# Kernel tuning notes

Hardware: AMD Instinct MI355X
Metric: run time of the kernel (lower is better)

## Reference

```python
import jax, jax.numpy as jnp
import numpy as np

COMMA_ID = 1010   # BERT wordpiece id for ','
H, NH, HD = 768, 8, 96
B, S = 64, 512
NSEG = 17         # 16 commas per row -> 17 segments
EPS = 1e-5


def setup_inputs() -> dict:
    key = jax.random.key(0)
    ks = jax.random.split(key, 16)
    text_hs = jax.random.normal(ks[0], (B, S, H), jnp.float32)
    cols_hs = jax.random.normal(ks[1], (B, S, H), jnp.float32)
    ids = jax.random.randint(ks[2], (B, S), 0, 30522)
    ids = jnp.where(ids == COMMA_ID, COMMA_ID + 1, ids)  # avoid accidental commas
    comma_pos = jnp.arange(16, 257, 16)                  # 16 commas per row
    ids = ids.at[:, comma_pos].set(COMMA_ID)
    sc = 0.02
    wq = jax.random.normal(ks[3], (H, H), jnp.float32) * sc
    wk = jax.random.normal(ks[4], (H, H), jnp.float32) * sc
    wv = jax.random.normal(ks[5], (H, H), jnp.float32) * sc
    bq = jnp.zeros((H,), jnp.float32)
    bk = jnp.zeros((H,), jnp.float32)
    bv = jnp.zeros((H,), jnp.float32)
    wo = jax.random.normal(ks[6], (H, H), jnp.float32) * sc
    bo = jnp.zeros((H,), jnp.float32)
    gamma = jnp.ones((H,), jnp.float32)
    beta = jnp.zeros((H,), jnp.float32)
    w_out = jax.random.normal(ks[7], (1, H), jnp.float32) * sc
    b_out = jnp.zeros((1,), jnp.float32)
    return dict(text_hs=text_hs, cols_hs=cols_hs, wq=wq, wk=wk, wv=wv,
                bq=bq, bk=bk, bv=bv, wo=wo, bo=bo, gamma=gamma, beta=beta,
                w_out=w_out, b_out=b_out, columns_input_ids=ids, n_segments=NSEG)


def _forward(text_hs, cols_hs, wq, wk, wv, bq, bk, bv, wo, bo,
             gamma, beta, w_out, b_out, columns_input_ids, n_segments):
    t = text_hs[:, 1:, :]   # drop first token, as in forward()  [B, L, H]
    c = cols_hs[:, 1:, :]
    L = t.shape[1]
    # --- nn.MultiheadAttention(query=cols, key=value=text), batch_first ---
    q = c @ wq.T + bq
    k = t @ wk.T + bk
    v = t @ wv.T + bv
    split = lambda x: x.reshape(x.shape[0], -1, NH, HD).transpose(0, 2, 1, 3)
    scores = jnp.einsum('bhqd,bhkd->bhqk', split(q), split(k)) / np.sqrt(HD).astype(np.float32)
    attn = jax.nn.softmax(scores, axis=-1)
    ctx = jnp.einsum('bhqk,bhkd->bhqd', attn, split(v))
    ctx = ctx.transpose(0, 2, 1, 3).reshape(c.shape[0], L, H)
    attn_out = ctx @ wo.T + bo
    # --- BatchNorm1d over channels (training-mode batch stats) ---
    xt = attn_out.transpose(0, 2, 1)            # [B, H, L]
    mu = xt.mean(axis=(0, 2), keepdims=True)
    var = xt.var(axis=(0, 2), keepdims=True)     # biased, as torch BN normalization
    xn = (xt - mu) / jnp.sqrt(var + EPS) * gamma[None, :, None] + beta[None, :, None]
    cross_out = c + xn.transpose(0, 2, 1)       # residual add
    fv = (cross_out @ w_out.T + b_out).squeeze(-1)   # [B, L] scores per token
    # --- compose_outputs: mean-pool comma-delimited ragged spans ---
    is_comma = columns_input_ids[:, :L] == COMMA_ID
    seg = jnp.cumsum(is_comma.astype(jnp.int32), axis=1) - is_comma.astype(jnp.int32)
    mask = (jnp.arange(L)[None, :] >= 1) & (~is_comma)    # slice_start=1, commas excluded
    oh = ((seg[:, :, None] == jnp.arange(n_segments)[None, None, :])
          & mask[:, :, None]).astype(fv.dtype)            # [B, L, J]
    sums = jnp.einsum('blj,bl->bj', oh, fv)
    cnt = oh.sum(axis=1)
    return sums / jnp.maximum(cnt, 1.0)                   # [B, n_segments]


def reference(text_hs, cols_hs, wq, wk, wv, bq, bk, bv, wo, bo,
              gamma, beta, w_out, b_out, columns_input_ids, n_segments):
    return _forward(text_hs, cols_hs, wq, wk, wv, bq, bk, bv, wo, bo,
                    gamma, beta, w_out, b_out, columns_input_ids, n_segments)
```

## Files before the change

kernel.cpp:

```cpp
#include <hip/hip_runtime.h>
#include <hip/hip_bf16.h>

#define COMMA_IDC 1010
#define NHEAD 8
#define Ll 511
#define Mrows 32704
#define NSEG 17

typedef __attribute__((ext_vector_type(8))) short bf16x8;
typedef __attribute__((ext_vector_type(4))) float f32x4;
typedef unsigned short u16;
typedef unsigned int u32;
typedef unsigned long long u64;

__device__ __forceinline__ u16 f2b(float f) {
  __hip_bfloat16 h = __float2bfloat16(f);
  return *reinterpret_cast<u16*>(&h);
}
__device__ __forceinline__ float b2f(u16 u) {
  u32 x = ((u32)u) << 16;
  return __builtin_bit_cast(float, x);
}

__device__ __forceinline__ void gld_lds16(const void* g, void* l) {
  __builtin_amdgcn_global_load_lds(
      (const __attribute__((address_space(1))) void*)(u64)g,
      (__attribute__((address_space(3))) void*)(u32)(u64)l,
      16, 0, 0);
}

#define MFMA16(a, b, c) __builtin_amdgcn_mfma_f32_16x16x32_bf16(a, b, c, 0, 0, 0)

__global__ void conv_sliced2(const float4* __restrict__ s0, const float4* __restrict__ s1,
                             ushort4* __restrict__ d0, ushort4* __restrict__ d1) {
  const float4* src = blockIdx.z ? s1 : s0;
  ushort4* dst = blockIdx.z ? d1 : d0;
  int b = blockIdx.y;
  int idx = blockIdx.x * 256 + threadIdx.x;
  if (idx >= Ll * 192) return;
  int l = idx / 192, c = idx - l * 192;
  float4 v = src[(b * 512 + l + 1) * 192 + c];
  ushort4 o; o.x = f2b(v.x); o.y = f2b(v.y); o.z = f2b(v.z); o.w = f2b(v.w);
  dst[(b * Ll + l) * 192 + c] = o;
}

__global__ void conv_w(const float4* __restrict__ wq, const float4* __restrict__ wk,
                       const float4* __restrict__ wv, const float4* __restrict__ wo,
                       ushort4* __restrict__ wqkvb, ushort4* __restrict__ wob) {
  int i = blockIdx.x * 256 + threadIdx.x;
  int seg = i / 147456, off = i - seg * 147456;
  const float4* s = (seg == 0) ? wq : ((seg == 1) ? wk : ((seg == 2) ? wv : wo));
  ushort4* d = (seg == 3) ? wob : (wqkvb + seg * 147456);
  float4 v = s[off];
  ushort4 o; o.x = f2b(v.x); o.y = f2b(v.y); o.z = f2b(v.z); o.w = f2b(v.w);
  d[off] = o;
}

__global__ void zero_kernel(float* p, int n) {
  int i = blockIdx.x * 256 + threadIdx.x;
  if (i < n) p[i] = 0.f;
}

#define LDA_(i, kk) (*(const bf16x8*)(sMem + bA + ((i) * 16 + fr) * 64 + ((((kk) * 4 + fq) ^ xm) << 3)))
#define LDW_(j, kk) (*(const bf16x8*)(sMem + bW + (((wc * 64 + (j) * 16) >> 7) * 8192) + \
                     (((wc * 64 + (j) * 16) & 127) + fr) * 64 + ((((kk) * 4 + fq) ^ xm) << 3)))
#define LGKM0 do { asm volatile("s_waitcnt lgkmcnt(0)" ::: "memory"); __builtin_amdgcn_sched_barrier(0); } while (0)

template<int NTILES, int NOUT, int QNT>
__global__ __launch_bounds__(512, 2) void gemm256(
    const u16* __restrict__ A0, const u16* __restrict__ A1, const u16* __restrict__ W,
    const float* __restrict__ b0, const float* __restrict__ b1, const float* __restrict__ b2,
    u16* __restrict__ outp)
{
  __shared__ __align__(16) u16 sMem[65536];
  const int tid = threadIdx.x;
  const int lane = tid & 63, wid = tid >> 6;
  const int fr = lane & 15, fq = lane >> 4;
  const int wr = wid >> 2, wc = wid & 3;
  const int xm = fr & 7;

  int fid = blockIdx.x;
  int xcd = fid & 7, w = fid >> 3;
  int mrow = xcd * 16 + w / NTILES;
  int ncol = w - (w / NTILES) * NTILES;
  const int m0 = mrow * 256, n0 = ncol * 256;
  const u16* __restrict__ A = (ncol < QNT) ? A0 : A1;

  const int rS = tid >> 3;
  const int cS = (tid & 7) ^ (rS & 7);
  const u16* gA0 = A + (u64)(m0 + rS) * 768 + cS * 8;
  const u16* gA1 = A + (u64)(m0 + 128 + rS) * 768 + cS * 8;
  const u16* gW0 = W + (u64)(n0 + rS) * 768 + cS * 8;
  const u16* gW1 = W + (u64)(n0 + 128 + rS) * 768 + cS * 8;
  const u32 st0 = tid * 8;

  f32x4 acc[8][4] = {};

  auto stage_all = [&](int buf, int kt) {
    const int kb = kt * 64;
    const u32 db = (u32)buf * 32768;
    gld_lds16(gA0 + kb, sMem + db + st0);
    gld_lds16(gA0 + kb + 49152, sMem + db + st0 + 4096);
    gld_lds16(gA1 + kb, sMem + db + 8192 + st0);
    gld_lds16(gA1 + kb + 49152, sMem + db + 8192 + st0 + 4096);
    gld_lds16(gW0 + kb, sMem + db + 16384 + st0);
    gld_lds16(gW0 + kb + 49152, sMem + db + 16384 + st0 + 4096);
    gld_lds16(gW1 + kb, sMem + db + 24576 + st0);
    gld_lds16(gW1 + kb + 49152, sMem + db + 24576 + st0 + 4096);
  };

  stage_all(0, 0);
  asm volatile("s_waitcnt vmcnt(0)" ::: "memory");
  __builtin_amdgcn_s_barrier();

  for (int kt = 0; kt < 12; ++kt) {
    const u32 db = (u32)(kt & 1) * 32768;
    const u32 bA = db + wr * 8192;
    const u32 bW = db + 16384;
    bf16x8 af[4][2], wf[2][2];

#pragma unroll
    for (int i = 0; i < 4; i++) { af[i][0] = LDA_(i, 0); af[i][1] = LDA_(i, 1); }
#pragma unroll
    for (int j = 0; j < 2; j++) { wf[j][0] = LDW_(j, 0); wf[j][1] = LDW_(j, 1); }
    __builtin_amdgcn_s_barrier();
    if (kt + 1 < 12) stage_all((kt + 1) & 1, kt + 1);
    LGKM0;
    __builtin_amdgcn_s_setprio(1);
#pragma unroll
    for (int i = 0; i < 4; i++)
#pragma unroll
      for (int j = 0; j < 2; j++) {
        acc[i][j] = MFMA16(af[i][0], wf[j][0], acc[i][j]);
        acc[i][j] = MFMA16(af[i][1], wf[j][1], acc[i][j]);
      }
    __builtin_amdgcn_s_setprio(0);
    __builtin_amdgcn_s_barrier();

#pragma unroll
    for (int j = 0; j < 2; j++) { wf[j][0] = LDW_(j + 2, 0); wf[j][1] = LDW_(j + 2, 1); }
    __builtin_amdgcn_s_barrier();
    LGKM0;
    __builtin_amdgcn_s_setprio(1);
#pragma unroll
    for (int i = 0; i < 4; i++)
#pragma unroll
      for (int j = 0; j < 2; j++) {
        acc[i][j + 2] = MFMA16(af[i][0], wf[j][0], acc[i][j + 2]);
        acc[i][j + 2] = MFMA16(af[i][1], wf[j][1], acc[i][j + 2]);
      }
    __builtin_amdgcn_s_setprio(0);
    __builtin_amdgcn_s_barrier();

#pragma unroll
    for (int i = 0; i < 4; i++) { af[i][0] = LDA_(i + 4, 0); af[i][1] = LDA_(i + 4, 1); }
#pragma unroll
    for (int j = 0; j < 2; j++) { wf[j][0] = LDW_(j, 0); wf[j][1] = LDW_(j, 1); }
    __builtin_amdgcn_s_barrier();
    LGKM0;
    __builtin_amdgcn_s_setprio(1);
#pragma unroll
    for (int i = 0; i < 4; i++)
#pragma unroll
      for (int j = 0; j < 2; j++) {
        acc[i + 4][j] = MFMA16(af[i][0], wf[j][0], acc[i + 4][j]);
        acc[i + 4][j] = MFMA16(af[i][1], wf[j][1], acc[i + 4][j]);
      }
    __builtin_amdgcn_s_setprio(0);
    __builtin_amdgcn_s_barrier();

#pragma unroll
    for (int j = 0; j < 2; j++) { wf[j][0] = LDW_(j + 2, 0); wf[j][1] = LDW_(j + 2, 1); }
    __builtin_amdgcn_s_barrier();
    LGKM0;
    __builtin_amdgcn_s_setprio(1);
#pragma unroll
    for (int i = 0; i < 4; i++)
#pragma unroll
      for (int j = 0; j < 2; j++) {
        acc[i + 4][j + 2] = MFMA16(af[i][0], wf[j][0], acc[i + 4][j + 2]);
        acc[i + 4][j + 2] = MFMA16(af[i][1], wf[j][1], acc[i + 4][j + 2]);
      }
    __builtin_amdgcn_s_setprio(0);
    asm volatile("s_waitcnt vmcnt(0)" ::: "memory");
    __builtin_amdgcn_s_barrier();
  }

  const float* bp = (n0 < 768) ? b0 : ((n0 < 1536) ? b1 : b2);
  const int bcol = n0 & 767;
  float bj[4];
#pragma unroll
  for (int j = 0; j < 4; j++) bj[j] = bp[bcol + wc * 64 + j * 16 + fr];

#pragma unroll
  for (int h = 0; h < 2; h++) {
    __syncthreads();
    if (wr == h) {
#pragma unroll
      for (int i = 0; i < 8; i++)
#pragma unroll
        for (int j = 0; j < 4; j++)
#pragma unroll
          for (int r = 0; r < 4; r++)
            sMem[(i * 16 + fq * 4 + r) * 264 + wc * 64 + j * 16 + fr] = f2b(acc[i][j][r] + bj[j]);
    }
    __syncthreads();
#pragma unroll
    for (int it = 0; it < 8; it++) {
      int chunk = tid + it * 512;
      int lr = chunk >> 5, ch = chunk & 31;
      *(bf16x8*)(outp + (u64)(m0 + h * 128 + lr) * NOUT + n0 + ch * 8) =
          *(const bf16x8*)(sMem + lr * 264 + ch * 8);
    }
  }
}

__global__ __launch_bounds__(256) void vtrans(const u16* __restrict__ QKV, u16* __restrict__ VT) {
  __shared__ __align__(16) u16 sT[128 * 128];
  int bh = blockIdx.y;
  int b = bh >> 3, h = bh & 7;
  int l0 = blockIdx.x * 128;
  u16* outp = VT + (u64)bh * 96 * 512;
  int t = threadIdx.x;
#pragma unroll
  for (int k = 0; k < 6; k++) {
    int c = t + k * 256;
    int l = c / 12, ch = c - l * 12;
    int lc = l0 + l; if (lc > 510) lc = 510;
    bf16x8 v = *(const bf16x8*)(QKV + (u64)(b * 511 + lc) * 2304 + 1536 + h * 96 + ch * 8);
    int chunk = l * 16 + (ch ^ ((l >> 3) & 7));
    *(bf16x8*)(sT + chunk * 8) = v;
  }
  __syncthreads();
#pragma unroll
  for (int k = 0; k < 6; k++) {
    int c = t + k * 256;
    int d = c >> 4, lch = c & 15;
    u16 vals[8];
#pragma unroll
    for (int k2 = 0; k2 < 8; k2++) {
      int r = lch * 8 + k2;
      int idx = r * 128 + (((d >> 3) ^ (lch & 7)) << 3) + (d & 7);
      vals[k2] = sT[idx];
    }
    bf16x8 o;
#pragma unroll
    for (int k2 = 0; k2 < 8; k2++) o[k2] = (short)vals[k2];
    *(bf16x8*)(outp + (u64)d * 512 + l0 + lch * 8) = o;
  }
}

#define PST 36
__global__ __launch_bounds__(256) void attn_kernel(
    const u16* __restrict__ QKV, const u16* __restrict__ VT, u16* __restrict__ ctxb)
{
  __shared__ __align__(16) u16 sK[32 * 96];
  __shared__ __align__(16) u16 sV[32 * 96];
  __shared__ __align__(16) u16 sP[4][16 * PST];
  const int tid = threadIdx.x, lane = tid & 63, wid = tid >> 6;
  int fid = blockIdx.x;
  int xcd = fid & 7, slot = (fid >> 3) & 3, grp = fid >> 5;
  int bh = grp * 8 + xcd;
  int b = bh >> 3, h = bh & 7;
  int q0 = slot * 128;
  const int fr = lane & 15, fq = lane >> 4;
  const u64 mb = (u64)(b * 511);
  const u64 hbV = (u64)bh * 96 * 512;

  bf16x8 qf[2][3];
#pragma unroll
  for (int sub = 0; sub < 2; sub++) {
    int qr = q0 + wid * 32 + sub * 16 + fr; if (qr > 510) qr = 510;
#pragma unroll
    for (int ks = 0; ks < 3; ks++)
      qf[sub][ks] = *(const bf16x8*)(QKV + (mb + qr) * 2304 + h * 96 + ks * 32 + fq * 8);
  }

  f32x4 ctx[2][6] = {};
  f32x4 sumP[2] = {};

  int cK1 = wid * 64 + lane;
  int kr1 = cK1 / 12, kc1 = cK1 - kr1 * 12;
  const u16* gK1 = QKV + (mb + kr1) * 2304 + 768 + h * 96 + kc1 * 8;
  int cK2 = 256 + cK1;
  int kr2 = cK2 / 12, kc2 = cK2 - kr2 * 12;
  const u16* gK2 = QKV + (mb + kr2) * 2304 + 768 + h * 96 + kc2 * 8;
  int cV1 = wid * 64 + lane;
  int dV1 = cV1 >> 2, jV1 = (cV1 & 3) ^ ((dV1 >> 1) & 3);
  const u16* gV1 = VT + hbV + (u64)dV1 * 512 + jV1 * 8;
  int cV2 = 256 + (wid - 2) * 64 + lane;
  int dV2 = cV2 >> 2, jV2 = (cV2 & 3) ^ ((dV2 >> 1) & 3);
  const u16* gV2 = VT + hbV + (u64)dV2 * 512 + jV2 * 8;

  u16* lK1 = sK + (u32)(wid * 64) * 8;
  u16* lK2 = sK + (u32)(256 + wid * 64) * 8;
  u16* lV1 = sV + (u32)(wid * 64) * 8;
  u16* lV2 = sV + (u32)(256 + (wid - 2) * 64) * 8;
  u16* pw = &sP[wid][0];

  const float cs = 0.10206207261596575f;
  const int cpx = fq ^ ((fr >> 1) & 3);

  for (int kv0 = 0; kv0 < 511; kv0 += 32) {
    __syncthreads();
    gld_lds16(gK1, lK1); gK1 += (u64)32 * 2304;
    if (wid < 2) { gld_lds16(gK2, lK2); gK2 += (u64)32 * 2304; }
    gld_lds16(gV1, lV1); gV1 += 32;
    if (wid >= 2) { gld_lds16(gV2, lV2); gV2 += 32; }
    __syncthreads();

    bf16x8 kf0[3], kf1[3];
#pragma unroll
    for (int ks = 0; ks < 3; ks++) {
      kf0[ks] = *(const bf16x8*)(sK + fr * 96 + ks * 32 + fq * 8);
      kf1[ks] = *(const bf16x8*)(sK + (16 + fr) * 96 + ks * 32 + fq * 8);
    }
    const bool ok1 = (kv0 + 16 + fr) < Ll;

#pragma unroll
    for (int sub = 0; sub < 2; sub++) {
      f32x4 s0 = {}, s1 = {};
#pragma unroll
      for (int ks = 0; ks < 3; ks++) {
        s0 = MFMA16(qf[sub][ks], kf0[ks], s0);
        s1 = MFMA16(qf[sub][ks], kf1[ks], s1);
      }
      float p0[4], p1[4];
#pragma unroll
      for (int r = 0; r < 4; r++) {
        p0[r] = __expf(s0[r] * cs);
        float e1 = __expf(s1[r] * cs);
        p1[r] = ok1 ? e1 : 0.f;
        sumP[sub][r] += p0[r] + p1[r];
      }
#pragma unroll
      for (int r = 0; r < 4; r++) {
        int row = fq * 4 + r;
        pw[row * PST + fr] = f2b(p0[r]);
        pw[row * PST + 16 + fr] = f2b(p1[r]);
      }
      bf16x8 pf = *(const bf16x8*)(pw + fr * PST + fq * 8);
#pragma unroll
      for (int df = 0; df < 6; df++) {
        bf16x8 vf = *(const bf16x8*)(sV + (df * 16 + fr) * 32 + cpx * 8);
        ctx[sub][df] = MFMA16(pf, vf, ctx[sub][df]);
      }
    }
  }

#pragma unroll
  for (int sub = 0; sub < 2; sub++) {
    float inv[4];
#pragma unroll
    for (int r = 0; r < 4; r++) {
      float s = sumP[sub][r];
      s += __shfl_xor(s, 1, 64);
      s += __shfl_xor(s, 2, 64);
      s += __shfl_xor(s, 4, 64);
      s += __shfl_xor(s, 8, 64);
      inv[r] = 1.f / s;
    }
#pragma unroll
    for (int df = 0; df < 6; df++) {
#pragma unroll
      for (int r = 0; r < 4; r++) {
        int q = q0 + wid * 32 + sub * 16 + fq * 4 + r;
        if (q < Ll)
          ctxb[(u64)(b * Ll + q) * 768 + h * 96 + df * 16 + fr] = f2b(ctx[sub][df][r] * inv[r]);
      }
    }
  }
}

__global__ __launch_bounds__(256) void stats_kernel(const u16* __restrict__ ao,
                                                    float* __restrict__ ssum, float* __restrict__ ssq)
{
  int t = threadIdx.x;
  int row0 = blockIdx.x * 128;
  int rowEnd = row0 + 128; if (rowEnd > Mrows) rowEnd = Mrows;
  float s[3] = {0.f, 0.f, 0.f}, q[3] = {0.f, 0.f, 0.f};
  for (int m = row0; m < rowEnd; m++) {
    const u16* rp = ao + (u64)m * 768;
#pragma unroll
    for (int i = 0; i < 3; i++) {
      float v = b2f(rp[t + i * 256]);
      s[i] += v; q[i] += v * v;
    }
  }
#pragma unroll
  for (int i = 0; i < 3; i++) {
    atomicAdd(&ssum[t + i * 256], s[i]);
    atomicAdd(&ssq[t + i * 256], q[i]);
  }
}

__global__ __launch_bounds__(256) void derived_kernel(
    const float* __restrict__ ssum, const float* __restrict__ ssq,
    const float* __restrict__ w_out, const float* __restrict__ b_out,
    const float* __restrict__ gamma, const float* __restrict__ beta,
    float* __restrict__ weff, float* __restrict__ consts)
{
  __shared__ float red[256];
  int t = threadIdx.x;
  float acc = 0.f;
  const float invN = 1.f / 32704.f;
#pragma unroll
  for (int i = 0; i < 3; i++) {
    int hh = t + i * 256;
    float mu = ssum[hh] * invN;
    float var = ssq[hh] * invN - mu * mu;
    float rstd = 1.f / sqrtf(var + 1e-5f);
    float we = w_out[hh] * gamma[hh] * rstd;
    weff[hh] = we;
    acc += w_out[hh] * beta[hh] - we * mu;
  }
  red[t] = acc; __syncthreads();
  for (int s = 128; s > 0; s >>= 1) { if (t < s) red[t] += red[t + s]; __syncthreads(); }
  if (t == 0) consts[0] = b_out[0] + red[0];
}

__global__ __launch_bounds__(256) void fv_kernel(
    const u16* __restrict__ ao, const u16* __restrict__ cb,
    const float* __restrict__ w_out, const float* __restrict__ weff,
    const float* __restrict__ consts, float* __restrict__ fv)
{
  int lane = threadIdx.x & 63, wid = threadIdx.x >> 6;
  int m = blockIdx.x * 4 + wid;
  if (m >= Mrows) return;
  const u16* ap = ao + (u64)m * 768;
  const u16* cp = cb + (u64)m * 768;
  float acc = 0.f;
#pragma unroll
  for (int i = 0; i < 12; i++) {
    int hh = lane + i * 64;
    acc += b2f(ap[hh]) * weff[hh] + b2f(cp[hh]) * w_out[hh];
  }
#pragma unroll
  for (int off = 1; off < 64; off <<= 1) acc += __shfl_xor(acc, off, 64);
  if (lane == 0) fv[m] = acc + consts[0];
}

__global__ __launch_bounds__(64) void seg_kernel(
    const float* __restrict__ fv, const int* __restrict__ ids, float* __restrict__ out)
{
  __shared__ float ssum[NSEG];
  __shared__ int scnt[NSEG];
  int lane = threadIdx.x;
  int b = blockIdx.x;
  if (lane < NSEG) { ssum[lane] = 0.f; scnt[lane] = 0; }
  __syncthreads();
  int carry = 0;
  for (int it = 0; it < 8; it++) {
    int l = it * 64 + lane;
    bool active = l < Ll;
    int id = active ? ids[b * 512 + l] : 0;
    bool comma = active && (id == COMMA_IDC);
    u64 cmask = __ballot(comma);
    int seg = carry + __popcll(cmask & ((1ull << lane) - 1ull));
    bool valid = active && (l >= 1) && !comma;
    if (valid && seg < NSEG) {
      atomicAdd(&ssum[seg], fv[b * Ll + l]);
      atomicAdd(&scnt[seg], 1);
    }
    carry += __popcll(cmask);
  }
  __syncthreads();
  if (lane < NSEG) {
    float c = (float)scnt[lane];
    out[b * NSEG + lane] = ssum[lane] / fmaxf(c, 1.f);
  }
}

extern "C" void kernel_launch(void* const* d_in, const int* in_sizes, int n_in,
                              void* d_out, int out_size, void* d_ws, size_t ws_size,
                              hipStream_t stream)
{
  const float* text  = (const float*)d_in[0];
  const float* cols  = (const float*)d_in[1];
  const float* wq    = (const float*)d_in[2];
  const float* wk    = (const float*)d_in[3];
  const float* wvp   = (const float*)d_in[4];
  const float* bq    = (const float*)d_in[5];
  const float* bk    = (const float*)d_in[6];
  const float* bv    = (const float*)d_in[7];
  const float* wo    = (const float*)d_in[8];
  const float* bo    = (const float*)d_in[9];
  const float* gamma = (const float*)d_in[10];
  const float* beta  = (const float*)d_in[11];
  const float* w_out = (const float*)d_in[12];
  const float* b_out = (const float*)d_in[13];
  const int*   ids   = (const int*)d_in[14];
  float* out = (float*)d_out;

  char* ws = (char*)d_ws;
  u16* cb    = (u16*)(ws + 0ull);
  u16* tb    = (u16*)(ws + 50331648ull);
  u16* wqkvb = (u16*)(ws + 100663296ull);
  u16* wob   = (u16*)(ws + 104202240ull);
  u16* QKVb  = (u16*)(ws + 105381888ull);
  u16* ctxb  = (u16*)(ws + 256376832ull);
  u16* VTb   = tb;
  u16* aob   = QKVb;
  float* ssum   = (float*)(ws + 105381888ull + 50331648ull);
  float* ssq    = ssum + 768;
  float* weff   = ssum + 1536;
  float* consts = ssum + 2304;
  float* fv     = (float*)((char*)ssum + 16384ull);

  conv_sliced2<<<dim3(384, 64, 2), 256, 0, stream>>>(
      (const float4*)cols, (const float4*)text, (ushort4*)cb, (ushort4*)tb);
  conv_w<<<2304, 256, 0, stream>>>(
      (const float4*)wq, (const float4*)wk, (const float4*)wvp, (const float4*)wo,
      (ushort4*)wqkvb, (ushort4*)wob);

  gemm256<9, 2304, 3><<<1152, 512, 0, stream>>>(cb, tb, wqkvb, bq, bk, bv, QKVb);
  vtrans<<<dim3(4, 512), 256, 0, stream>>>(QKVb, VTb);
  attn_kernel<<<2048, 256, 0, stream>>>(QKVb, VTb, ctxb);

  zero_kernel<<<6, 256, 0, stream>>>(ssum, 1536);
  gemm256<3, 768, 99><<<384, 512, 0, stream>>>(ctxb, ctxb, wob, bo, bo, bo, aob);
  stats_kernel<<<256, 256, 0, stream>>>(aob, ssum, ssq);
  derived_kernel<<<1, 256, 0, stream>>>(ssum, ssq, w_out, b_out, gamma, beta, weff, consts);
  fv_kernel<<<8176, 256, 0, stream>>>(aob, cb, w_out, weff, consts, fv);
  seg_kernel<<<64, 64, 0, stream>>>(fv, ids, out);
}
```

Before: 460.2 us.

## Software-pipeline GEMM LDS fragment loads with MFMA using double register sets

Restructures the bf16 GEMM main loop so LDS fragment reads for the next sub-block are issued while MFMAs on the previous fragments run. Two register sets (A/B) are used, and the last quadrant's MFMAs are carried into the next iteration and an epilogue. Most per-quadrant s_barriers and explicit lgkmcnt waits are removed. The aim is to hide LDS latency and cut synchronisation stalls, at the cost of more VGPRs (possible spilling under launch bounds 512,2) and reliance on compiler-inserted waits.

```diff
diff --git a/kernel.cpp b/kernel.cpp
--- a/kernel.cpp
+++ b/kernel.cpp
@@ -30,6 +30,7 @@
 }
 
 #define MFMA16(a, b, c) __builtin_amdgcn_mfma_f32_16x16x32_bf16(a, b, c, 0, 0, 0)
+#define SBAR0 __builtin_amdgcn_sched_barrier(0)
 
 __global__ void conv_sliced2(const float4* __restrict__ s0, const float4* __restrict__ s1,
                              ushort4* __restrict__ d0, ushort4* __restrict__ d1) {
@@ -61,10 +62,9 @@
   if (i < n) p[i] = 0.f;
 }
 
-#define LDA_(i, kk) (*(const bf16x8*)(sMem + bA + ((i) * 16 + fr) * 64 + ((((kk) * 4 + fq) ^ xm) << 3)))
-#define LDW_(j, kk) (*(const bf16x8*)(sMem + bW + (((wc * 64 + (j) * 16) >> 7) * 8192) + \
+#define LDA(db, i, kk) (*(const bf16x8*)(sMem + (db) + wr * 8192 + ((i) * 16 + fr) * 64 + ((((kk) * 4 + fq) ^ xm) << 3)))
+#define LDW(db, j, kk) (*(const bf16x8*)(sMem + (db) + 16384 + (((wc * 64 + (j) * 16) >> 7) * 8192) + \
                      (((wc * 64 + (j) * 16) & 127) + fr) * 64 + ((((kk) * 4 + fq) ^ xm) << 3)))
-#define LGKM0 do { asm volatile("s_waitcnt lgkmcnt(0)" ::: "memory"); __builtin_amdgcn_sched_barrier(0); } while (0)
 
 template<int NTILES, int NOUT, int QNT>
 __global__ __launch_bounds__(512, 2) void gemm256(
@@ -95,6 +95,7 @@
   const u32 st0 = tid * 8;
 
   f32x4 acc[8][4] = {};
+  bf16x8 afA[4][2], afB[4][2], wfA[2][2], wfB[2][2];
 
   auto stage_all = [&](int buf, int kt) {
     const int kb = kt * 64;
@@ -110,80 +111,87 @@
   };
 
   stage_all(0, 0);
-  asm volatile("s_waitcnt vmcnt(0)" ::: "memory");
-  __builtin_amdgcn_s_barrier();
 
   for (int kt = 0; kt < 12; ++kt) {
     const u32 db = (u32)(kt & 1) * 32768;
-    const u32 bA = db + wr * 8192;
-    const u32 bW = db + 16384;
-    bf16x8 af[4][2], wf[2][2];
-
-#pragma unroll
-    for (int i = 0; i < 4; i++) { af[i][0] = LDA_(i, 0); af[i][1] = LDA_(i, 1); }
-#pragma unroll
-    for (int j = 0; j < 2; j++) { wf[j][0] = LDW_(j, 0); wf[j][1] = LDW_(j, 1); }
+
+    asm volatile("s_waitcnt vmcnt(0)" ::: "memory");
+    SBAR0;
     __builtin_amdgcn_s_barrier();
+    SBAR0;
+#pragma unroll
+    for (int i = 0; i < 4; i++) { afA[i][0] = LDA(db, i, 0); afA[i][1] = LDA(db, i, 1); }
+#pragma unroll
+    for (int j = 0; j < 2; j++) { wfA[j][0] = LDW(db, j, 0); wfA[j][1] = LDW(db, j, 1); }
+    if (kt > 0) {
+      __builtin_amdgcn_s_setprio(1);
+#pragma unroll
+      for (int i = 0; i < 4; i++)
+#pragma unroll
+        for (int j = 0; j < 2; j++) {
+          acc[i + 4][j + 2] = MFMA16(afB[i][0], wfB[j][0], acc[i + 4][j + 2]);
+          acc[i + 4][j + 2] = MFMA16(afB[i][1], wfB[j][1], acc[i + 4][j + 2]);
+        }
+      __builtin_amdgcn_s_setprio(0);
+    }
+    SBAR0;
+    __builtin_amdgcn_s_barrier();
+    SBAR0;
     if (kt + 1 < 12) stage_all((kt + 1) & 1, kt + 1);
-    LGKM0;
+    SBAR0;
+
+#pragma unroll
+    for (int j = 0; j < 2; j++) { wfB[j][0] = LDW(db, j + 2, 0); wfB[j][1] = LDW(db, j + 2, 1); }
     __builtin_amdgcn_s_setprio(1);
 #pragma unroll
     for (int i = 0; i < 4; i++)
 #pragma unroll
       for (int j = 0; j < 2; j++) {
-        acc[i][j] = MFMA16(af[i][0], wf[j][0], acc[i][j]);
-        acc[i][j] = MFMA16(af[i][1], wf[j][1], acc[i][j]);
+        acc[i][j] = MFMA16(afA[i][0], wfA[j][0], acc[i][j]);
+        acc[i][j] = MFMA16(afA[i][1], wfA[j][1], acc[i][j]);
       }
     __builtin_amdgcn_s_setprio(0);
-    __builtin_amdgcn_s_barrier();
-
-#pragma unroll
-    for (int j = 0; j < 2; j++) { wf[j][0] = LDW_(j + 2, 0); wf[j][1] = LDW_(j + 2, 1); }
-    __builtin_amdgcn_s_barrier();
-    LGKM0;
+    SBAR0;
+
+#pragma unroll
+    for (int i = 0; i < 4; i++) { afB[i][0] = LDA(db, i + 4, 0); afB[i][1] = LDA(db, i + 4, 1); }
+#pragma unroll
+    for (int j = 0; j < 2; j++) { wfA[j][0] = LDW(db, j, 0); wfA[j][1] = LDW(db, j, 1); }
     __builtin_amdgcn_s_setprio(1);
 #pragma unroll
     for (int i = 0; i < 4; i++)
 #pragma unroll
       for (int j = 0; j < 2; j++) {
-        acc[i][j + 2] = MFMA16(af[i][0], wf[j][0], acc[i][j + 2]);
-        acc[i][j + 2] = MFMA16(af[i][1], wf[j][1], acc[i][j + 2]);
+        acc[i][j + 2] = MFMA16(afA[i][0], wfB[j][0], acc[i][j + 2]);
+        acc[i][j + 2] = MFMA16(afA[i][1], wfB[j][1], acc[i][j + 2]);
       }
     __builtin_amdgcn_s_setprio(0);
-    __builtin_amdgcn_s_barrier();
-
-#pragma unroll
-    for (int i = 0; i < 4; i++) { af[i][0] = LDA_(i + 4, 0); af[i][1] = LDA_(i + 4, 1); }
-#pragma unroll
-    for (int j = 0; j < 2; j++) { wf[j][0] = LDW_(j, 0); wf[j][1] = LDW_(j, 1); }
-    __builtin_amdgcn_s_barrier();
-    LGKM0;
+    SBAR0;
+
+#pragma unroll
+    for (int j = 0; j < 2; j++) { wfB[j][0] = LDW(db, j + 2, 0); wfB[j][1] = LDW(db, j + 2, 1); }
     __builtin_amdgcn_s_setprio(1);
 #pragma unroll
     for (int i = 0; i < 4; i++)
 #pragma unroll
       for (int j = 0; j < 2; j++) {
-        acc[i + 4][j] = MFMA16(af[i][0], wf[j][0], acc[i + 4][j]);
-        acc[i + 4][j] = MFMA16(af[i][1], wf[j][1], acc[i + 4][j]);
+        acc[i + 4][j] = MFMA16(afB[i][0], wfA[j][0], acc[i + 4][j]);
+        acc[i + 4][j] = MFMA16(afB[i][1], wfA[j][1], acc[i + 4][j]);
       }
     __builtin_amdgcn_s_setprio(0);
-    __builtin_amdgcn_s_barrier();
-
-#pragma unroll
-    for (int j = 0; j < 2; j++) { wf[j][0] = LDW_(j + 2, 0); wf[j][1] = LDW_(j + 2, 1); }
-    __builtin_amdgcn_s_barrier();
-    LGKM0;
+    SBAR0;
+  }
+
+  {
     __builtin_amdgcn_s_setprio(1);
 #pragma unroll
     for (int i = 0; i < 4; i++)
 #pragma unroll
       for (int j = 0; j < 2; j++) {
-        acc[i + 4][j + 2] = MFMA16(af[i][0], wf[j][0], acc[i + 4][j + 2]);
-        acc[i + 4][j + 2] = MFMA16(af[i][1], wf[j][1], acc[i + 4][j + 2]);
+        acc[i + 4][j + 2] = MFMA16(afB[i][0], wfB[j][0], acc[i + 4][j + 2]);
+        acc[i + 4][j + 2] = MFMA16(afB[i][1], wfB[j][1], acc[i + 4][j + 2]);
       }
     __builtin_amdgcn_s_setprio(0);
-    asm volatile("s_waitcnt vmcnt(0)" ::: "memory");
-    __builtin_amdgcn_s_barrier();
   }
 
   const float* bp = (n0 < 768) ? b0 : ((n0 < 1536) ? b1 : b2);
```

After: 440.6 us. 4.2% less time.
